# Kernel optimization log

Hardware: AMD Instinct MI355X
Metric: run time of the kernel (lower is better)

## Reference

```python
import math
import jax, jax.numpy as jnp
from jax import lax
import numpy as np

B, CIN, COUT, K, SD, NCLS, H, W = 8, 512, 512, 3, 512, 35, 64, 64
EPS_DEMOD = 1e-8
EPS_IN = 1e-5  # torch InstanceNorm2d default eps


def _equal_linear(x, w, b):
    # EqualLinear: F.linear(x, w * (1/sqrt(in_dim))) + b  (lr_mul=1)
    return x @ (w.T * (1.0 / math.sqrt(w.shape[1]))) + b


def setup_inputs() -> dict:
    key = jax.random.key(0)
    ks = jax.random.split(key, 8)
    return {
        "input": jax.random.normal(ks[0], (B, CIN, H, W), jnp.float32),
        "style": jax.random.normal(ks[1], (B, SD), jnp.float32),
        "class_style": jax.random.normal(ks[2], (NCLS, SD), jnp.float32),
        "weight": jax.random.normal(ks[3], (1, COUT, CIN, K, K), jnp.float32),
        "mod_w": jax.random.normal(ks[4], (CIN, SD), jnp.float32),
        "mod_b": jnp.ones((CIN,), jnp.float32),  # bias_init=1
        "cw_w": jax.random.normal(ks[5], (COUT, SD), jnp.float32),
        "cw_b": jnp.ones((COUT,), jnp.float32),
        "cb_w": jax.random.normal(ks[6], (COUT, SD), jnp.float32),
        "cb_b": jnp.ones((COUT,), jnp.float32),
        "label_class_dict": jax.random.randint(ks[7], (B, H, W), 0, NCLS),
    }


def reference(input, style, class_style, weight, mod_w, mod_b, cw_w, cw_b, cb_w, cb_b, label_class_dict):
    scale = 1.0 / math.sqrt(CIN * K * K)
    pad = K // 2

    # per-sample style modulation of weights
    s = _equal_linear(style, mod_w, mod_b)                 # [B, CIN]
    w = scale * weight * s[:, None, :, None, None]         # [B, COUT, CIN, K, K]
    demod = lax.rsqrt(jnp.sum(w * w, axis=(2, 3, 4)) + EPS_DEMOD)  # [B, COUT]
    w = w * demod[:, :, None, None, None]

    # grouped conv (groups = batch) == vmap of per-sample conv
    def conv_one(x, wb):  # x [CIN,H,W], wb [COUT,CIN,K,K]
        return lax.conv_general_dilated(
            x[None], wb, window_strides=(1, 1), padding=[(pad, pad), (pad, pad)],
            dimension_numbers=("NCHW", "OIHW", "NCHW"))[0]

    out = jax.vmap(conv_one)(input, w)                     # [B, COUT, H, W]

    # param-free instance norm (biased variance, no affine)
    mu = out.mean(axis=(2, 3), keepdims=True)
    var = out.var(axis=(2, 3), keepdims=True)
    out = (out - mu) * lax.rsqrt(var + EPS_IN)

    # CLADE per-class affine from class_style, gathered via label map
    cw = _equal_linear(class_style, cw_w, cw_b)            # [NCLS, COUT]
    cb = _equal_linear(class_style, cb_w, cb_b)            # [NCLS, COUT]
    class_weight = jnp.transpose(cw[label_class_dict], (0, 3, 1, 2))  # [B,COUT,H,W]
    class_bias = jnp.transpose(cb[label_class_dict], (0, 3, 1, 2))
    return out * class_weight + class_bias
```

## Files before the change

### kernel.cpp

```cpp
#include <hip/hip_runtime.h>

typedef unsigned short u16;
typedef unsigned int u32;
typedef __attribute__((ext_vector_type(8))) short short8;
typedef __attribute__((ext_vector_type(4))) float floatx4;

__device__ inline float bf2f(u16 h) {
  union { u32 u; float f; } v; v.u = ((u32)h) << 16; return v.f;
}
__device__ inline u16 f2bf(float f) {
  union { float f; u32 u; } v; v.f = f;
  u32 u = v.u;
  return (u16)((u + 0x7fffu + ((u >> 16) & 1u)) >> 16);
}
__device__ inline float ldf(const void* p, int i, int isbf) {
  return isbf ? bf2f(((const u16*)p)[i]) : ((const float*)p)[i];
}

__global__ __launch_bounds__(256) void prep_kernel(
    const void* __restrict__ style, const void* __restrict__ class_style,
    const void* __restrict__ weight,
    const void* __restrict__ mod_w, const void* __restrict__ mod_b,
    const void* __restrict__ cw_w, const void* __restrict__ cw_b,
    const void* __restrict__ cb_w, const void* __restrict__ cb_b,
    const void* __restrict__ x,
    float* __restrict__ s, float* __restrict__ cw, float* __restrict__ cb,
    u16* __restrict__ wT, float* __restrict__ wsqT2, u16* __restrict__ xT) {
  __shared__ float smem[4608];
  __shared__ int cnt;
  const int t = threadIdx.x;

  if (t == 0) cnt = 0;
  __syncthreads();
  {
    u32 v = ((const u32*)weight)[1024 + t];
    int e = (v >> 7) & 0xFF;
    if (e >= 96 && e <= 160) atomicAdd(&cnt, 1);
  }
  __syncthreads();
  const int isbf = (cnt >= 154) ? 1 : 0;
  const int bid = blockIdx.x;

  if (bid < 78) {
    int row = bid;
    const void *vec, *wm, *bias; float* out; int voff;
    if (row < 8)        { vec = style;       voff = row*512;      wm = mod_w; bias = mod_b; out = s  + row*512; }
    else if (row < 43)  { vec = class_style; voff = (row-8)*512;  wm = cw_w;  bias = cw_b;  out = cw + (row-8)*512; }
    else                { vec = class_style; voff = (row-43)*512; wm = cb_w;  bias = cb_b;  out = cb + (row-43)*512; }
    float* v = smem;
    for (int i = t; i < 512; i += 256) v[i] = ldf(vec, voff + i, isbf);
    __syncthreads();
    const float inv = 0.04419417382415922f;
    for (int o = t; o < 512; o += 256) {
      float acc = 0.f;
      if (isbf) {
        for (int k = 0; k < 512; ++k) acc += bf2f(((const u16*)wm)[o*512 + k]) * v[k];
      } else {
        const float4* wr = (const float4*)((const float*)wm + o*512);
        for (int k = 0; k < 128; ++k) {
          float4 p = wr[k];
          acc += p.x*v[k*4+0] + p.y*v[k*4+1] + p.z*v[k*4+2] + p.w*v[k*4+3];
        }
      }
      out[o] = acc * inv + ldf(bias, o, isbf);
    }
  } else if (bid < 590) {
    const int co = bid - 78;
    float* wsmem = smem;
    for (int i = t; i < 4608; i += 256)
      wsmem[i] = ldf(weight, co*4608 + i, isbf);
    __syncthreads();
    for (int ci = t; ci < 512; ci += 256) {
      float sq = 0.f;
      const int ck = ci >> 5, cin = ci & 31;
      #pragma unroll
      for (int tap = 0; tap < 9; ++tap) {
        float fv = wsmem[ci*9 + tap];
        sq += fv*fv;
        wT[(size_t)(((ck*9 + tap)*512) + co)*32 + cin] = f2bf(fv);
      }
      wsqT2[(size_t)co*512 + ci] = sq;
    }
  } else {
    const int r = bid - 590;
    const int ck = r & 15, h = (r >> 4) & 63, b = r >> 10;
    float* sv = smem;
    float* sl = smem + 512;
    for (int i = t; i < 512; i += 256) sv[i] = ldf(style, b*512 + i, isbf);
    __syncthreads();
    const int lane = t & 63, wv = t >> 6;
    const float inv = 0.04419417382415922f;
    #pragma unroll
    for (int p = 0; p < 8; ++p) {
      const int row = p*4 + wv;
      const int ci = ck*32 + row;
      float partial = 0.f;
      if (isbf) {
        const u16* wr = (const u16*)mod_w + (size_t)ci*512 + lane*8;
        #pragma unroll
        for (int k = 0; k < 8; ++k) partial += bf2f(wr[k]) * sv[lane*8 + k];
      } else {
        const float4* wr = (const float4*)((const float*)mod_w + (size_t)ci*512 + lane*8);
        float4 p0 = wr[0], p1 = wr[1];
        partial += p0.x*sv[lane*8+0] + p0.y*sv[lane*8+1] + p0.z*sv[lane*8+2] + p0.w*sv[lane*8+3]
                 + p1.x*sv[lane*8+4] + p1.y*sv[lane*8+5] + p1.z*sv[lane*8+6] + p1.w*sv[lane*8+7];
      }
      #pragma unroll
      for (int off = 1; off < 64; off <<= 1) partial += __shfl_xor(partial, off, 64);
      if (lane == 0) sl[row] = partial * inv + ldf(mod_b, ci, isbf);
    }
    __syncthreads();
    const int w = t & 63, cq = t >> 6;
    float f[8];
    #pragma unroll
    for (int j = 0; j < 8; ++j) {
      float xv = ldf(x, (((b*512) + ck*32 + cq*8 + j)*64 + h)*64 + w, isbf);
      f[j] = xv * sl[cq*8 + j];
    }
    u32 outp[4];
    #pragma unroll
    for (int i = 0; i < 4; ++i)
      outp[i] = (u32)f2bf(f[2*i]) | ((u32)f2bf(f[2*i+1]) << 16);
    uint4 po = {outp[0], outp[1], outp[2], outp[3]};
    *(uint4*)&xT[(size_t)((((b*16 + ck)*64 + h)*64 + w)*32) + cq*8] = po;
  }
}

__global__ __launch_bounds__(256, 2) void conv_kernel(const u16* __restrict__ xT, const u16* __restrict__ wT,
                                                      float* __restrict__ y, float* __restrict__ part) {
  __shared__ __align__(16) u16 xs[10*4*66*8];
  __shared__ __align__(16) u16 wsm[9*4*64*8];
  const int tid = threadIdx.x;
  const int lane = tid & 63;
  const int wid = tid >> 6;
  const int hb = blockIdx.x, b = blockIdx.y;
  const int ct0 = blockIdx.z * 64;
  const int h0 = hb * 8;

  if (tid < 80) {
    int q = tid / 20, rem = tid % 20, dr = rem >> 1, side = rem & 1;
    uint4 z = {0,0,0,0};
    *(uint4*)&xs[(((dr*4 + q)*66) + side*65)*8] = z;
  }

  floatx4 acc[4][8];
  #pragma unroll
  for (int i = 0; i < 4; ++i) {
    #pragma unroll
    for (int j = 0; j < 8; ++j) acc[i][j] = (floatx4)(0.f);
  }

  const int m = lane & 15, qd = lane >> 4;

  for (int ck = 0; ck < 16; ++ck) {
    __syncthreads();

    #pragma unroll
    for (int j = 0; j < 10; ++j) {
      int g = tid + j*256;
      int q = g & 3, c64 = (g >> 2) & 63, dr = g >> 8;
      int hin = h0 + dr - 1;
      uint4 v = {0,0,0,0};
      if (hin >= 0 && hin <= 63)
        v = *(const uint4*)&xT[(size_t)((((b*16 + ck)*64 + hin)*64 + c64)*32) + q*8];
      *(uint4*)&xs[(((dr*4 + q)*66) + 1 + c64)*8] = v;
    }
    #pragma unroll
    for (int j = 0; j < 9; ++j) {
      int g = tid + j*256;
      int q = g & 3, co = (g >> 2) & 63, tap = g >> 8;
      uint4 v = *(const uint4*)&wT[(size_t)(((ck*9 + tap)*512) + ct0 + co)*32 + q*8];
      *(uint4*)&wsm[(((tap*4 + q)*64) + (co ^ (q << 1)))*8] = v;
    }
    __syncthreads();

    #pragma unroll
    for (int tap = 0; tap < 9; ++tap) {
      const int k1 = tap / 3, k2 = tap - k1*3;
      short8 af[4], bfr[8];
      #pragma unroll
      for (int mi = 0; mi < 4; ++mi)
        af[mi] = *(const short8*)&wsm[(((tap*4 + qd)*64) + ((mi*16 + m) ^ (qd << 1)))*8];
      #pragma unroll
      for (int hh = 0; hh < 2; ++hh) {
        const int dr = wid*2 + hh + k1;
        #pragma unroll
        for (int nw = 0; nw < 4; ++nw)
          bfr[hh*4 + nw] = *(const short8*)&xs[(((dr*4 + qd)*66) + nw*16 + m + k2)*8];
      }
      #pragma unroll
      for (int ni = 0; ni < 8; ++ni) {
        #pragma unroll
        for (int mi = 0; mi < 4; ++mi)
          acc[mi][ni] = __builtin_amdgcn_mfma_f32_16x16x32_bf16(af[mi], bfr[ni], acc[mi][ni], 0, 0, 0);
      }
    }
  }

  #pragma unroll
  for (int mi = 0; mi < 4; ++mi) {
    #pragma unroll
    for (int hh = 0; hh < 2; ++hh) {
      const int h = h0 + wid*2 + hh;
      #pragma unroll
      for (int nw = 0; nw < 4; ++nw) {
        #pragma unroll
        for (int r = 0; r < 4; ++r) {
          int co = ct0 + mi*16 + qd*4 + r;
          int w = nw*16 + m;
          y[(size_t)(((b*512) + co)*64 + h)*64 + w] = acc[mi][hh*4 + nw][r];
        }
      }
    }
  }

  float s1[16], s2[16];
  #pragma unroll
  for (int mi = 0; mi < 4; ++mi) {
    #pragma unroll
    for (int r = 0; r < 4; ++r) {
      float a = 0.f, aa = 0.f;
      #pragma unroll
      for (int ni = 0; ni < 8; ++ni) {
        float v = acc[mi][ni][r];
        a += v; aa += v*v;
      }
      s1[mi*4+r] = a; s2[mi*4+r] = aa;
    }
  }
  #pragma unroll
  for (int off = 1; off < 16; off <<= 1) {
    #pragma unroll
    for (int i = 0; i < 16; ++i) {
      s1[i] += __shfl_xor(s1[i], off, 64);
      s2[i] += __shfl_xor(s2[i], off, 64);
    }
  }
  __syncthreads();
  float* red = (float*)xs;
  if (m == 0) {
    #pragma unroll
    for (int mi = 0; mi < 4; ++mi) {
      #pragma unroll
      for (int r = 0; r < 4; ++r) {
        int co = mi*16 + qd*4 + r;
        red[(wid*64 + co)*2 + 0] = s1[mi*4+r];
        red[(wid*64 + co)*2 + 1] = s2[mi*4+r];
      }
    }
  }
  __syncthreads();
  if (tid < 128) {
    int co = tid >> 1, which = tid & 1;
    float v = (red[(0*64+co)*2+which] + red[(1*64+co)*2+which])
            + (red[(2*64+co)*2+which] + red[(3*64+co)*2+which]);
    part[(size_t)(((b*8 + hb)*512) + ct0 + co)*2 + which] = v;
  }
}

__global__ __launch_bounds__(256) void epi_kernel(float* __restrict__ y, const float* __restrict__ part,
                                                  const float* __restrict__ s, const float* __restrict__ wsqT2,
                                                  const float* __restrict__ cw, const float* __restrict__ cb,
                                                  const int* __restrict__ label) {
  const int bc = blockIdx.x;
  const int b = bc >> 9, co = bc & 511;
  const int t = threadIdx.x;
  __shared__ float tabw[35], tabb[35];
  __shared__ float redp[4];
  __shared__ float2 msh;
  if (t < 35) { tabw[t] = cw[t*512 + co]; tabb[t] = cb[t*512 + co]; }

  const float* sb = s + b*512;
  const float* wq = wsqT2 + (size_t)co*512;
  float ep;
  {
    float s0 = sb[t], s1v = sb[t + 256];
    ep = s0*s0*wq[t] + s1v*s1v*wq[t + 256];
  }
  #pragma unroll
  for (int off = 1; off < 64; off <<= 1) ep += __shfl_xor(ep, off, 64);
  if ((t & 63) == 0) redp[t >> 6] = ep;
  __syncthreads();
  if (t == 0) {
    float SS = redp[0] + redp[1] + redp[2] + redp[3];
    float S = 0.f, Q = 0.f;
    const float2* pv = (const float2*)part;
    #pragma unroll
    for (int hb = 0; hb < 8; ++hb) {
      float2 p = pv[(size_t)((b*8 + hb)*512) + co];
      S += p.x; Q += p.y;
    }
    float mval = S * (1.f/4096.f);
    float var = fmaxf(Q * (1.f/4096.f) - mval*mval, 0.f);
    float eps = 1e-5f*SS + 4.608e-10f;
    msh = make_float2(mval, rsqrtf(var + eps));
  }
  __syncthreads();
  const float mval = msh.x, is = msh.y;

  float* yp = y + (size_t)bc*4096 + t*16;
  const int* lp = label + b*4096 + t*16;
  #pragma unroll
  for (int u = 0; u < 4; ++u) {
    float4 v = *(const float4*)(yp + u*4);
    int4 l = *(const int4*)(lp + u*4);
    float4 o;
    o.x = (v.x - mval)*is*tabw[l.x] + tabb[l.x];
    o.y = (v.y - mval)*is*tabw[l.y] + tabb[l.y];
    o.z = (v.z - mval)*is*tabw[l.z] + tabb[l.z];
    o.w = (v.w - mval)*is*tabw[l.w] + tabb[l.w];
    *(float4*)(yp + u*4) = o;
  }
}

extern "C" void kernel_launch(void* const* d_in, const int* in_sizes, int n_in,
                              void* d_out, int out_size, void* d_ws, size_t ws_size,
                              hipStream_t stream) {
  (void)in_sizes; (void)n_in; (void)out_size; (void)ws_size;
  const void* input       = d_in[0];
  const void* style       = d_in[1];
  const void* class_style = d_in[2];
  const void* weight      = d_in[3];
  const void* mod_w       = d_in[4];
  const void* mod_b       = d_in[5];
  const void* cw_w        = d_in[6];
  const void* cw_b        = d_in[7];
  const void* cb_w        = d_in[8];
  const void* cb_b        = d_in[9];
  const int* label        = (const int*)d_in[10];
  float* y = (float*)d_out;

  char* ws = (char*)d_ws;
  u16*   xT    = (u16*)  (ws + 0);
  u16*   wT    = (u16*)  (ws + 33554432);
  float* wsqT2 = (float*)(ws + 38273024);
  float* s     = (float*)(ws + 39321600);
  float* cw    = (float*)(ws + 39337984);
  float* cb    = (float*)(ws + 39409664);
  float* part  = (float*)(ws + 39481344);

  hipLaunchKernelGGL(prep_kernel, dim3(8782), dim3(256), 0, stream,
                     style, class_style, weight, mod_w, mod_b, cw_w, cw_b, cb_w, cb_b,
                     input, s, cw, cb, wT, wsqT2, xT);
  hipLaunchKernelGGL(conv_kernel, dim3(8, 8, 8), dim3(256), 0, stream, xT, wT, y, part);
  hipLaunchKernelGGL(epi_kernel, dim3(4096), dim3(256), 0, stream, y, part, s, wsqT2, cw, cb, label);
}
```

Baseline: 330.9 us.

## Double-buffer conv LDS tiles via direct global-to-LDS loads with 512-thread blocks

Reorders the xT and wT workspace layouts so that each 64-lane wave can copy a contiguous 16-byte-per-lane slab straight into LDS with global_load_lds. The conv kernel now double-buffers the input and weight tiles, prefetching the next channel chunk while MFMAs run on the current one. Blocks grow to 512 threads, each wave handling one output row, so per-thread accumulators are halved. The cost is about twice the LDS per block, which can limit occupancy. The XOR swizzle on the weight tile is dropped, which may bring back LDS bank conflicts.

New measurement: 340.8 us. +3.0%, slower.

```diff
diff --git a/kernel.cpp b/kernel.cpp
--- a/kernel.cpp
+++ b/kernel.cpp
@@ -5,6 +5,9 @@
 typedef __attribute__((ext_vector_type(8))) short short8;
 typedef __attribute__((ext_vector_type(4))) float floatx4;
 
+typedef const u32 __attribute__((address_space(1))) glb_u32;
+typedef u32 __attribute__((address_space(3))) lds_u32;
+
 __device__ inline float bf2f(u16 h) {
   union { u32 u; float f; } v; v.u = ((u32)h) << 16; return v.f;
 }
@@ -15,6 +18,9 @@
 }
 __device__ inline float ldf(const void* p, int i, int isbf) {
   return isbf ? bf2f(((const u16*)p)[i]) : ((const float*)p)[i];
+}
+__device__ inline void gl16(const void* g, void* l) {
+  __builtin_amdgcn_global_load_lds((glb_u32*)g, (lds_u32*)l, 16, 0, 0);
 }
 
 __global__ __launch_bounds__(256) void prep_kernel(
@@ -66,18 +72,19 @@
     }
   } else if (bid < 590) {
     const int co = bid - 78;
+    const int ctb = co >> 6, col = co & 63;
     float* wsmem = smem;
     for (int i = t; i < 4608; i += 256)
       wsmem[i] = ldf(weight, co*4608 + i, isbf);
     __syncthreads();
     for (int ci = t; ci < 512; ci += 256) {
       float sq = 0.f;
-      const int ck = ci >> 5, cin = ci & 31;
+      const int ck = ci >> 5, q = (ci >> 3) & 3, e = ci & 7;
       #pragma unroll
       for (int tap = 0; tap < 9; ++tap) {
         float fv = wsmem[ci*9 + tap];
         sq += fv*fv;
-        wT[(size_t)(((ck*9 + tap)*512) + co)*32 + cin] = f2bf(fv);
+        wT[((size_t)(ck*8 + ctb)*2304 + (tap*4 + q)*64 + col)*8 + e] = f2bf(fv);
       }
       wsqT2[(size_t)co*512 + ci] = sq;
     }
@@ -122,93 +129,101 @@
     for (int i = 0; i < 4; ++i)
       outp[i] = (u32)f2bf(f[2*i]) | ((u32)f2bf(f[2*i+1]) << 16);
     uint4 po = {outp[0], outp[1], outp[2], outp[3]};
-    *(uint4*)&xT[(size_t)((((b*16 + ck)*64 + h)*64 + w)*32) + cq*8] = po;
-  }
-}
-
-__global__ __launch_bounds__(256, 2) void conv_kernel(const u16* __restrict__ xT, const u16* __restrict__ wT,
+    *(uint4*)&xT[((size_t)(((b*16 + ck)*64 + h)*256) + t)*8] = po;
+  }
+}
+
+__global__ __launch_bounds__(512, 2) void conv_kernel(const u16* __restrict__ xT, const u16* __restrict__ wT,
                                                       float* __restrict__ y, float* __restrict__ part) {
-  __shared__ __align__(16) u16 xs[10*4*66*8];
-  __shared__ __align__(16) u16 wsm[9*4*64*8];
+  __shared__ __align__(16) u16 xs[2*2680*8];
+  __shared__ __align__(16) u16 wsm[2*2304*8];
   const int tid = threadIdx.x;
   const int lane = tid & 63;
   const int wid = tid >> 6;
   const int hb = blockIdx.x, b = blockIdx.y;
-  const int ct0 = blockIdx.z * 64;
+  const int ctb = blockIdx.z;
+  const int ct0 = ctb * 64;
   const int h0 = hb * 8;
-
-  if (tid < 80) {
-    int q = tid / 20, rem = tid % 20, dr = rem >> 1, side = rem & 1;
+  const int m = lane & 15, qd = lane >> 4;
+
+  {
     uint4 z = {0,0,0,0};
-    *(uint4*)&xs[(((dr*4 + q)*66) + side*65)*8] = z;
-  }
-
-  floatx4 acc[4][8];
+    for (int i = tid; i < 5360; i += 512) *(uint4*)&xs[i*8] = z;
+  }
+
+  floatx4 acc[4][4];
   #pragma unroll
   for (int i = 0; i < 4; ++i) {
     #pragma unroll
-    for (int j = 0; j < 8; ++j) acc[i][j] = (floatx4)(0.f);
-  }
-
-  const int m = lane & 15, qd = lane >> 4;
+    for (int j = 0; j < 4; ++j) acc[i][j] = (floatx4)(0.f);
+  }
+  __syncthreads();
+
+  #define STAGE(bn, ckn)                                                                   \
+    {                                                                                      \
+      u16* xb = &xs[(bn)*21440];                                                           \
+      u16* wb = &wsm[(bn)*18432];                                                          \
+      for (int sl = wid; sl < 76; sl += 8) {                                               \
+        if (sl < 40) {                                                                     \
+          int dr = sl >> 2, q = sl & 3;                                                    \
+          int hin = h0 + dr - 1;                                                           \
+          if (hin >= 0 && hin <= 63) {                                                     \
+            const u16* src = xT + ((size_t)(((b*16 + (ckn))*64 + hin)*256 + q*64 + lane))*8;\
+            gl16(src, &xb[((dr*4 + q)*67 + 1)*8]);                                         \
+          }                                                                                \
+        } else {                                                                           \
+          int j = sl - 40;                                                                 \
+          const u16* src = wT + ((size_t)(((ckn)*8 + ctb)*2304 + j*64 + lane))*8;          \
+          gl16(src, &wb[(j*64)*8]);                                                        \
+        }                                                                                  \
+      }                                                                                    \
+    }
+
+  STAGE(0, 0);
+  asm volatile("s_waitcnt vmcnt(0)" ::: "memory");
+  __syncthreads();
 
   for (int ck = 0; ck < 16; ++ck) {
-    __syncthreads();
-
-    #pragma unroll
-    for (int j = 0; j < 10; ++j) {
-      int g = tid + j*256;
-      int q = g & 3, c64 = (g >> 2) & 63, dr = g >> 8;
-      int hin = h0 + dr - 1;
-      uint4 v = {0,0,0,0};
-      if (hin >= 0 && hin <= 63)
-        v = *(const uint4*)&xT[(size_t)((((b*16 + ck)*64 + hin)*64 + c64)*32) + q*8];
-      *(uint4*)&xs[(((dr*4 + q)*66) + 1 + c64)*8] = v;
-    }
-    #pragma unroll
-    for (int j = 0; j < 9; ++j) {
-      int g = tid + j*256;
-      int q = g & 3, co = (g >> 2) & 63, tap = g >> 8;
-      uint4 v = *(const uint4*)&wT[(size_t)(((ck*9 + tap)*512) + ct0 + co)*32 + q*8];
-      *(uint4*)&wsm[(((tap*4 + q)*64) + (co ^ (q << 1)))*8] = v;
-    }
-    __syncthreads();
-
+    const int buf = ck & 1;
+    if (ck < 15) STAGE(buf ^ 1, ck + 1);
+
+    const u16* xb = &xs[buf*21440];
+    const u16* wb = &wsm[buf*18432];
     #pragma unroll
     for (int tap = 0; tap < 9; ++tap) {
       const int k1 = tap / 3, k2 = tap - k1*3;
-      short8 af[4], bfr[8];
+      const int dr = wid + k1;
+      short8 af[4], bfr[4];
       #pragma unroll
       for (int mi = 0; mi < 4; ++mi)
-        af[mi] = *(const short8*)&wsm[(((tap*4 + qd)*64) + ((mi*16 + m) ^ (qd << 1)))*8];
-      #pragma unroll
-      for (int hh = 0; hh < 2; ++hh) {
-        const int dr = wid*2 + hh + k1;
-        #pragma unroll
-        for (int nw = 0; nw < 4; ++nw)
-          bfr[hh*4 + nw] = *(const short8*)&xs[(((dr*4 + qd)*66) + nw*16 + m + k2)*8];
-      }
-      #pragma unroll
-      for (int ni = 0; ni < 8; ++ni) {
+        af[mi] = *(const short8*)&wb[((tap*4 + qd)*64 + mi*16 + m)*8];
+      #pragma unroll
+      for (int nw = 0; nw < 4; ++nw)
+        bfr[nw] = *(const short8*)&xb[((dr*4 + qd)*67 + nw*16 + m + k2)*8];
+      #pragma unroll
+      for (int nw = 0; nw < 4; ++nw) {
         #pragma unroll
         for (int mi = 0; mi < 4; ++mi)
-          acc[mi][ni] = __builtin_amdgcn_mfma_f32_16x16x32_bf16(af[mi], bfr[ni], acc[mi][ni], 0, 0, 0);
-      }
-    }
-  }
-
-  #pragma unroll
-  for (int mi = 0; mi < 4; ++mi) {
-    #pragma unroll
-    for (int hh = 0; hh < 2; ++hh) {
-      const int h = h0 + wid*2 + hh;
+          acc[mi][nw] = __builtin_amdgcn_mfma_f32_16x16x32_bf16(af[mi], bfr[nw], acc[mi][nw], 0, 0, 0);
+      }
+    }
+
+    asm volatile("s_waitcnt vmcnt(0)" ::: "memory");
+    __syncthreads();
+  }
+  #undef STAGE
+
+  {
+    const int h = h0 + wid;
+    #pragma unroll
+    for (int mi = 0; mi < 4; ++mi) {
       #pragma unroll
       for (int nw = 0; nw < 4; ++nw) {
         #pragma unroll
         for (int r = 0; r < 4; ++r) {
           int co = ct0 + mi*16 + qd*4 + r;
           int w = nw*16 + m;
-          y[(size_t)(((b*512) + co)*64 + h)*64 + w] = acc[mi][hh*4 + nw][r];
+          y[(size_t)(((b*512) + co)*64 + h)*64 + w] = acc[mi][nw][r];
         }
       }
     }
@@ -221,8 +236,8 @@
     for (int r = 0; r < 4; ++r) {
       float a = 0.f, aa = 0.f;
       #pragma unroll
-      for (int ni = 0; ni < 8; ++ni) {
-        float v = acc[mi][ni][r];
+      for (int nw = 0; nw < 4; ++nw) {
+        float v = acc[mi][nw][r];
         a += v; aa += v*v;
       }
       s1[mi*4+r] = a; s2[mi*4+r] = aa;
@@ -236,7 +251,6 @@
       s2[i] += __shfl_xor(s2[i], off, 64);
     }
   }
-  __syncthreads();
   float* red = (float*)xs;
   if (m == 0) {
     #pragma unroll
@@ -252,8 +266,9 @@
   __syncthreads();
   if (tid < 128) {
     int co = tid >> 1, which = tid & 1;
-    float v = (red[(0*64+co)*2+which] + red[(1*64+co)*2+which])
-            + (red[(2*64+co)*2+which] + red[(3*64+co)*2+which]);
+    float v = 0.f;
+    #pragma unroll
+    for (int w8 = 0; w8 < 8; ++w8) v += red[(w8*64 + co)*2 + which];
     part[(size_t)(((b*8 + hb)*512) + ct0 + co)*2 + which] = v;
   }
 }
@@ -342,6 +357,6 @@
   hipLaunchKernelGGL(prep_kernel, dim3(8782), dim3(256), 0, stream,
                      style, class_style, weight, mod_w, mod_b, cw_w, cw_b, cb_w, cb_b,
                      input, s, cw, cb, wT, wsqT2, xT);
-  hipLaunchKernelGGL(conv_kernel, dim3(8, 8, 8), dim3(256), 0, stream, xT, wT, y, part);
+  hipLaunchKernelGGL(conv_kernel, dim3(8, 8, 8), dim3(512), 0, stream, xT, wT, y, part);
   hipLaunchKernelGGL(epi_kernel, dim3(4096), dim3(256), 0, stream, y, part, s, wsqT2, cw, cb, label);
 }
```

## Use direct global-to-LDS loads with double-buffered weights and larger conv tiles

Applied to the files above, without the earlier changes.

The conv kernel now loads input and weight tiles with global_load_lds, copying straight from global memory into shared memory without passing through registers. Weight tiles are double-buffered so the next channel chunk is prefetched while the current one computes. The block grows to 512 threads covering 16 rows, which halves the grid and the partial-stat slots. The prep kernel writes xT and wT in layouts that match these direct LDS copies; the XOR swizzle is replaced by padding, which risks LDS bank conflicts on the weight reads and lowers occupancy because of the larger LDS footprint.

Measured after the change: 326.0 us. No clear change (-1.5%).

```diff
diff --git a/kernel.cpp b/kernel.cpp
--- a/kernel.cpp
+++ b/kernel.cpp
@@ -5,6 +5,9 @@
 typedef __attribute__((ext_vector_type(8))) short short8;
 typedef __attribute__((ext_vector_type(4))) float floatx4;
 
+typedef const u32 __attribute__((address_space(1))) glb_u32;
+typedef u32 __attribute__((address_space(3))) lds_u32;
+
 __device__ inline float bf2f(u16 h) {
   union { u32 u; float f; } v; v.u = ((u32)h) << 16; return v.f;
 }
@@ -15,6 +18,9 @@
 }
 __device__ inline float ldf(const void* p, int i, int isbf) {
   return isbf ? bf2f(((const u16*)p)[i]) : ((const float*)p)[i];
+}
+__device__ inline void gl16(const void* g, void* l) {
+  __builtin_amdgcn_global_load_lds((glb_u32*)g, (lds_u32*)l, 16, 0, 0);
 }
 
 __global__ __launch_bounds__(256) void prep_kernel(
@@ -66,18 +72,19 @@
     }
   } else if (bid < 590) {
     const int co = bid - 78;
+    const int ctb = co >> 6, col = co & 63;
     float* wsmem = smem;
     for (int i = t; i < 4608; i += 256)
       wsmem[i] = ldf(weight, co*4608 + i, isbf);
     __syncthreads();
     for (int ci = t; ci < 512; ci += 256) {
       float sq = 0.f;
-      const int ck = ci >> 5, cin = ci & 31;
+      const int ck = ci >> 5, q = (ci >> 3) & 3, e = ci & 7;
       #pragma unroll
       for (int tap = 0; tap < 9; ++tap) {
         float fv = wsmem[ci*9 + tap];
         sq += fv*fv;
-        wT[(size_t)(((ck*9 + tap)*512) + co)*32 + cin] = f2bf(fv);
+        wT[((size_t)(ck*8 + ctb)*2304 + (tap*4 + q)*64 + col)*8 + e] = f2bf(fv);
       }
       wsqT2[(size_t)co*512 + ci] = sq;
     }
@@ -122,25 +129,26 @@
     for (int i = 0; i < 4; ++i)
       outp[i] = (u32)f2bf(f[2*i]) | ((u32)f2bf(f[2*i+1]) << 16);
     uint4 po = {outp[0], outp[1], outp[2], outp[3]};
-    *(uint4*)&xT[(size_t)((((b*16 + ck)*64 + h)*64 + w)*32) + cq*8] = po;
-  }
-}
-
-__global__ __launch_bounds__(256, 2) void conv_kernel(const u16* __restrict__ xT, const u16* __restrict__ wT,
+    *(uint4*)&xT[((size_t)(((b*16 + ck)*64 + h)*256) + t)*8] = po;
+  }
+}
+
+__global__ __launch_bounds__(512, 2) void conv_kernel(const u16* __restrict__ xT, const u16* __restrict__ wT,
                                                       float* __restrict__ y, float* __restrict__ part) {
-  __shared__ __align__(16) u16 xs[10*4*66*8];
-  __shared__ __align__(16) u16 wsm[9*4*64*8];
+  __shared__ __align__(16) u16 xs[18*4*67*8];
+  __shared__ __align__(16) u16 wsm[2*2304*8];
   const int tid = threadIdx.x;
   const int lane = tid & 63;
   const int wid = tid >> 6;
-  const int hb = blockIdx.x, b = blockIdx.y;
-  const int ct0 = blockIdx.z * 64;
-  const int h0 = hb * 8;
-
-  if (tid < 80) {
-    int q = tid / 20, rem = tid % 20, dr = rem >> 1, side = rem & 1;
+  const int bid = blockIdx.x;
+  const int b = bid & 7, ctb = (bid >> 3) & 7, hb = bid >> 6;
+  const int ct0 = ctb * 64;
+  const int h0 = hb * 16;
+  const int m = lane & 15, qd = lane >> 4;
+
+  {
     uint4 z = {0,0,0,0};
-    *(uint4*)&xs[(((dr*4 + q)*66) + side*65)*8] = z;
+    for (int i = tid; i < 4824; i += 512) *(uint4*)&xs[i*8] = z;
   }
 
   floatx4 acc[4][8];
@@ -150,43 +158,48 @@
     for (int j = 0; j < 8; ++j) acc[i][j] = (floatx4)(0.f);
   }
 
-  const int m = lane & 15, qd = lane >> 4;
+  #define STAGE_X(ckn)                                                                     \
+    for (int sl = wid; sl < 72; sl += 8) {                                                 \
+      int dr = sl >> 2, q = sl & 3;                                                        \
+      int hin = h0 + dr - 1;                                                               \
+      if (hin >= 0 && hin <= 63) {                                                         \
+        const u16* src = xT + ((size_t)(((b*16 + (ckn))*64 + hin)*256 + q*64 + lane))*8;   \
+        gl16(src, &xs[((dr*4 + q)*67 + 1)*8]);                                             \
+      }                                                                                    \
+    }
+  #define STAGE_W(ckn, bn)                                                                 \
+    for (int j = wid; j < 36; j += 8) {                                                    \
+      const u16* src = wT + ((size_t)(((ckn)*8 + ctb)*2304 + j*64 + lane))*8;              \
+      gl16(src, &wsm[((bn)*2304 + j*64)*8]);                                               \
+    }
+
+  __syncthreads();
+  STAGE_W(0, 0);
 
   for (int ck = 0; ck < 16; ++ck) {
-    __syncthreads();
-
-    #pragma unroll
-    for (int j = 0; j < 10; ++j) {
-      int g = tid + j*256;
-      int q = g & 3, c64 = (g >> 2) & 63, dr = g >> 8;
-      int hin = h0 + dr - 1;
-      uint4 v = {0,0,0,0};
-      if (hin >= 0 && hin <= 63)
-        v = *(const uint4*)&xT[(size_t)((((b*16 + ck)*64 + hin)*64 + c64)*32) + q*8];
-      *(uint4*)&xs[(((dr*4 + q)*66) + 1 + c64)*8] = v;
-    }
-    #pragma unroll
-    for (int j = 0; j < 9; ++j) {
-      int g = tid + j*256;
-      int q = g & 3, co = (g >> 2) & 63, tap = g >> 8;
-      uint4 v = *(const uint4*)&wT[(size_t)(((ck*9 + tap)*512) + ct0 + co)*32 + q*8];
-      *(uint4*)&wsm[(((tap*4 + q)*64) + (co ^ (q << 1)))*8] = v;
-    }
-    __syncthreads();
-
+    const int buf = ck & 1;
+    __syncthreads();
+
+    STAGE_X(ck);
+    asm volatile("s_waitcnt vmcnt(0)" ::: "memory");
+    __syncthreads();
+
+    if (ck < 15) STAGE_W(ck + 1, buf ^ 1);
+
+    const u16* wb = &wsm[buf*2304*8];
     #pragma unroll
     for (int tap = 0; tap < 9; ++tap) {
       const int k1 = tap / 3, k2 = tap - k1*3;
       short8 af[4], bfr[8];
       #pragma unroll
       for (int mi = 0; mi < 4; ++mi)
-        af[mi] = *(const short8*)&wsm[(((tap*4 + qd)*64) + ((mi*16 + m) ^ (qd << 1)))*8];
+        af[mi] = *(const short8*)&wb[((tap*4 + qd)*64 + mi*16 + m)*8];
       #pragma unroll
       for (int hh = 0; hh < 2; ++hh) {
         const int dr = wid*2 + hh + k1;
         #pragma unroll
         for (int nw = 0; nw < 4; ++nw)
-          bfr[hh*4 + nw] = *(const short8*)&xs[(((dr*4 + qd)*66) + nw*16 + m + k2)*8];
+          bfr[hh*4 + nw] = *(const short8*)&xs[((dr*4 + qd)*67 + nw*16 + m + k2)*8];
       }
       #pragma unroll
       for (int ni = 0; ni < 8; ++ni) {
@@ -196,6 +209,8 @@
       }
     }
   }
+  #undef STAGE_X
+  #undef STAGE_W
 
   #pragma unroll
   for (int mi = 0; mi < 4; ++mi) {
@@ -252,9 +267,10 @@
   __syncthreads();
   if (tid < 128) {
     int co = tid >> 1, which = tid & 1;
-    float v = (red[(0*64+co)*2+which] + red[(1*64+co)*2+which])
-            + (red[(2*64+co)*2+which] + red[(3*64+co)*2+which]);
-    part[(size_t)(((b*8 + hb)*512) + ct0 + co)*2 + which] = v;
+    float v = 0.f;
+    #pragma unroll
+    for (int w8 = 0; w8 < 8; ++w8) v += red[(w8*64 + co)*2 + which];
+    part[(size_t)(((b*4 + hb)*512) + ct0 + co)*2 + which] = v;
   }
 }
 
@@ -286,8 +302,8 @@
     float S = 0.f, Q = 0.f;
     const float2* pv = (const float2*)part;
     #pragma unroll
-    for (int hb = 0; hb < 8; ++hb) {
-      float2 p = pv[(size_t)((b*8 + hb)*512) + co];
+    for (int hb = 0; hb < 4; ++hb) {
+      float2 p = pv[(size_t)((b*4 + hb)*512) + co];
       S += p.x; Q += p.y;
     }
     float mval = S * (1.f/4096.f);
@@ -342,6 +358,6 @@
   hipLaunchKernelGGL(prep_kernel, dim3(8782), dim3(256), 0, stream,
                      style, class_style, weight, mod_w, mod_b, cw_w, cw_b, cb_w, cb_b,
                      input, s, cw, cb, wT, wsqT2, xT);
-  hipLaunchKernelGGL(conv_kernel, dim3(8, 8, 8), dim3(256), 0, stream, xT, wT, y, part);
+  hipLaunchKernelGGL(conv_kernel, dim3(256), dim3(512), 0, stream, xT, wT, y, part);
   hipLaunchKernelGGL(epi_kernel, dim3(4096), dim3(256), 0, stream, y, part, s, wsqT2, cw, cb, label);
 }
```
